# Kernel optimization log

Hardware: AMD Instinct MI355X
Metric: run time of the kernel (lower is better)

Reference implementation:

```python
import jax, jax.numpy as jnp
import numpy as np

EPS = 1e-5  # torch BatchNorm1d default eps

def _bn(y, gamma, beta):
    # training-mode BatchNorm1d over batch axis (biased variance), per timestep
    mu = jnp.mean(y, axis=0, keepdims=True)
    var = jnp.mean((y - mu) ** 2, axis=0, keepdims=True)
    return gamma * (y - mu) * jax.lax.rsqrt(var + EPS) + beta

def setup_inputs() -> dict:
    key = jax.random.key(0)
    ks = jax.random.split(key, 16)
    T, B, I, H = 512, 64, 512, 512
    s = 1.0 / np.sqrt(H)
    def w(k, shape):
        return jax.random.uniform(k, shape, jnp.float32, -s, s)
    return {
        "x": jax.random.normal(ks[0], (T, B, I), jnp.float32),
        "h0": jnp.zeros((1, B, H), jnp.float32),
        "W_z_w": w(ks[1], (H, H)), "W_z_b": w(ks[2], (H,)),
        "U_z_w": w(ks[3], (H, I)), "U_z_b": w(ks[4], (H,)),
        "W_r_w": w(ks[5], (H, H)), "W_r_b": w(ks[6], (H,)),
        "U_r_w": w(ks[7], (H, I)), "U_r_b": w(ks[8], (H,)),
        "W_h_w": w(ks[9], (H, H)), "W_h_b": w(ks[10], (H,)),
        "U_h_w": w(ks[11], (H, I)), "U_h_b": w(ks[12], (H,)),
        "bn_gamma": jnp.ones((H,), jnp.float32),
        "bn_beta": jnp.zeros((H,), jnp.float32),
    }

def reference(x, h0, W_z_w, W_z_b, U_z_w, U_z_b, W_r_w, W_r_b, U_r_w, U_r_b,
              W_h_w, W_h_b, U_h_w, U_h_b, bn_gamma, bn_beta):
    T, B, _ = x.shape
    H = h0.shape[-1]
    # precompute input projections for all timesteps (parallelizable part)
    uz = jnp.einsum('tbi,hi->tbh', x, U_z_w) + U_z_b  # [T,B,H]
    ur = jnp.einsum('tbi,hi->tbh', x, U_r_w) + U_r_b
    uh = jnp.einsum('tbi,hi->tbh', x, U_h_w) + U_h_b

    def step(h, inp):
        uz_t, ur_t, uh_t = inp
        z = jax.nn.sigmoid(h @ W_z_w.T + W_z_b + _bn(uz_t, bn_gamma, bn_beta))
        r = jax.nn.sigmoid(h @ W_r_w.T + W_r_b + _bn(ur_t, bn_gamma, bn_beta))
        new_state = jnp.tanh((r * h) @ W_h_w.T + W_h_b + _bn(uh_t, bn_gamma, bn_beta))
        h_new = (1.0 - z) * h + z * new_state
        return h_new, h_new

    _, hs = jax.lax.scan(step, h0[0], (uz, ur, uh))  # hs: [T,B,H]
    output = hs.reshape(T, B, 1, H)   # [T, B, directions=1, H]
    h_out = hs.reshape(1, T, B, H)    # faithful to torch code's final `h`
    return output, h_out
```

## Files before the change

kernel.cpp:

```cpp
#include <hip/hip_runtime.h>
#include <hip/hip_bf16.h>


using bf16x8 = __attribute__((ext_vector_type(8))) short;
using f32x4  = __attribute__((ext_vector_type(4))) float;
using fvec4  = __attribute__((ext_vector_type(4))) float;

#define NWG 32

static __device__ __forceinline__ unsigned short f2bf(float f) {
  union { float ff; unsigned int i; } v; v.ff = f;
  unsigned int x = v.i;
  x += 0x7fffu + ((x >> 16) & 1u);
  return (unsigned short)(x >> 16);
}
static __device__ __forceinline__ float h2f(unsigned short u) {
  union { unsigned short s; _Float16 h; } v; v.s = u; return (float)v.h;
}
static __device__ __forceinline__ unsigned short f2h(float f) {
  union { unsigned short s; _Float16 h; } v; v.h = (_Float16)f; return v.s;
}
static __device__ __forceinline__ float sigmoidf_(float x) {
  return 1.0f / (1.0f + __expf(-x));
}
static __device__ __forceinline__ float tanhf_(float x) {
  return 2.0f / (1.0f + __expf(-2.0f * x)) - 1.0f;
}

__global__ __launch_bounds__(256) void proj_gemm(
    const float* __restrict__ x,
    const float* __restrict__ Uz, const float* __restrict__ Ur,
    const float* __restrict__ Uh,
    const float* __restrict__ Wzb, const float* __restrict__ Wrb,
    const float* __restrict__ Whb,
    const float* __restrict__ gamma, const float* __restrict__ beta,
    unsigned short* __restrict__ ubz, unsigned short* __restrict__ ubr,
    unsigned short* __restrict__ ubh)
{
  const int mt = blockIdx.x, nt = blockIdx.y, mat = blockIdx.z;
  const float* U  = (mat == 0) ? Uz  : (mat == 1 ? Ur  : Uh);
  const float* Wb = (mat == 0) ? Wzb : (mat == 1 ? Wrb : Whb);
  unsigned short* uo = (mat == 0) ? ubz : (mat == 1 ? ubr : ubh);

  __shared__ short lA[4096];
  __shared__ short lB[4096];

  const int tid = threadIdx.x;
  const int wave = tid >> 6, lane = tid & 63;
  const int fl = lane & 15, kseg = lane >> 4;

  f32x4 acc[4];
  #pragma unroll
  for (int n = 0; n < 4; ++n) acc[n] = f32x4{0.f, 0.f, 0.f, 0.f};

  const float* xb = x + (size_t)mt * 64 * 512;
  const float* Ub = U + (size_t)nt * 64 * 512;

  for (int kt = 0; kt < 8; ++kt) {
    __syncthreads();
    #pragma unroll
    for (int c = 0; c < 2; ++c) {
      const int chunk = tid + 256 * c;
      const int row = chunk >> 3, kc = chunk & 7;
      const int lb = row * 128 + ((kc * 16) ^ ((row & 7) << 4));
      {
        const float* g = xb + (size_t)row * 512 + kt * 64 + kc * 8;
        fvec4 a0 = *(const fvec4*)g, a1 = *(const fvec4*)(g + 4);
        bf16x8 p;
        p[0] = (short)f2bf(a0[0]); p[1] = (short)f2bf(a0[1]);
        p[2] = (short)f2bf(a0[2]); p[3] = (short)f2bf(a0[3]);
        p[4] = (short)f2bf(a1[0]); p[5] = (short)f2bf(a1[1]);
        p[6] = (short)f2bf(a1[2]); p[7] = (short)f2bf(a1[3]);
        *(bf16x8*)((char*)lA + lb) = p;
      }
      {
        const float* g = Ub + (size_t)row * 512 + kt * 64 + kc * 8;
        fvec4 a0 = *(const fvec4*)g, a1 = *(const fvec4*)(g + 4);
        bf16x8 p;
        p[0] = (short)f2bf(a0[0]); p[1] = (short)f2bf(a0[1]);
        p[2] = (short)f2bf(a0[2]); p[3] = (short)f2bf(a0[3]);
        p[4] = (short)f2bf(a1[0]); p[5] = (short)f2bf(a1[1]);
        p[6] = (short)f2bf(a1[2]); p[7] = (short)f2bf(a1[3]);
        *(bf16x8*)((char*)lB + lb) = p;
      }
    }
    __syncthreads();
    #pragma unroll
    for (int kk = 0; kk < 2; ++kk) {
      const int ar = wave * 16 + fl;
      bf16x8 af = *(const bf16x8*)((char*)lA + ar * 128 +
                    ((kk * 64 + kseg * 16) ^ ((ar & 7) << 4)));
      #pragma unroll
      for (int n = 0; n < 4; ++n) {
        const int br = n * 16 + fl;
        bf16x8 bfr = *(const bf16x8*)((char*)lB + br * 128 +
                      ((kk * 64 + kseg * 16) ^ ((br & 7) << 4)));
        acc[n] = __builtin_amdgcn_mfma_f32_16x16x32_bf16(af, bfr, acc[n], 0, 0, 0);
      }
    }
  }

  float sn[4], qn[4];
  #pragma unroll
  for (int n = 0; n < 4; ++n) {
    sn[n] = acc[n][0] + acc[n][1] + acc[n][2] + acc[n][3];
    qn[n] = acc[n][0]*acc[n][0] + acc[n][1]*acc[n][1]
          + acc[n][2]*acc[n][2] + acc[n][3]*acc[n][3];
    sn[n] += __shfl_xor(sn[n], 16); qn[n] += __shfl_xor(qn[n], 16);
    sn[n] += __shfl_xor(sn[n], 32); qn[n] += __shfl_xor(qn[n], 32);
  }
  __syncthreads();
  float* sArr = (float*)lA;
  float* qArr = (float*)lB;
  if (kseg == 0) {
    #pragma unroll
    for (int n = 0; n < 4; ++n) {
      sArr[wave * 64 + n * 16 + fl] = sn[n];
      qArr[wave * 64 + n * 16 + fl] = qn[n];
    }
  }
  __syncthreads();

  const int c0 = nt * 64;
  const int r0 = mt * 64 + wave * 16 + kseg * 4;
  #pragma unroll
  for (int n = 0; n < 4; ++n) {
    const int idx = n * 16 + fl;
    const float s = sArr[idx] + sArr[64+idx] + sArr[128+idx] + sArr[192+idx];
    const float q = qArr[idx] + qArr[64+idx] + qArr[128+idx] + qArr[192+idx];
    const float mu = s * 0.015625f;
    const float rs = rsqrtf(q * 0.015625f - mu * mu + 1e-5f);
    const int col = c0 + idx;
    const float gb  = gamma[col] * rs;
    const float ofs = beta[col] + Wb[col] - gb * mu;
    #pragma unroll
    for (int i = 0; i < 4; ++i)
      uo[(size_t)(r0 + i) * 512 + col] = f2h(gb * acc[n][i] + ofs);
  }
}

__global__ __launch_bounds__(256) void gru_scan(
    const float* __restrict__ h0,
    const float* __restrict__ Wz, const float* __restrict__ Wr,
    const float* __restrict__ Wh,
    const unsigned short* __restrict__ ubz, const unsigned short* __restrict__ ubr,
    const unsigned short* __restrict__ ubh,
    unsigned short* __restrict__ hbuf, unsigned short* __restrict__ rhbuf,
    unsigned int* __restrict__ bars, float* __restrict__ out)
{
  const int wg = blockIdx.x;
  const int tid = threadIdx.x;
  const int wave = tid >> 6, lane = tid & 63;
  const int fl = lane & 15, kseg = lane >> 4;
  const int col = wg * 16 + fl;
  const int row0 = wave * 16 + kseg * 4;
  const int hrow = wave * 16 + fl;

  __shared__ short lW[24576];

  for (int c = tid; c < 3072; c += 256) {
    const int m = c >> 10, rem = c & 1023;
    const int r = rem >> 6, kc = rem & 63;
    const float* W = (m == 0) ? Wz : (m == 1 ? Wr : Wh);
    const float* g = W + (size_t)(wg * 16 + r) * 512 + kc * 8;
    bf16x8 p;
    #pragma unroll
    for (int j = 0; j < 8; ++j) p[j] = (short)f2bf(g[j]);
    *(bf16x8*)((char*)lW + m * 16384 + r * 1024 + ((kc * 16) ^ ((r & 7) << 4))) = p;
  }

  float hown[4];
  #pragma unroll
  for (int i = 0; i < 4; ++i) {
    const float v = h0[(size_t)(row0 + i) * 512 + col];
    hown[i] = v;
    hbuf[(size_t)(row0 + i) * 512 + col] = f2bf(v);
  }
  __syncthreads();
  if (tid == 0)
    __hip_atomic_fetch_add(&bars[0], 1u, __ATOMIC_RELEASE, __HIP_MEMORY_SCOPE_AGENT);

  float uzv[4], urv[4], uhv[4];
  #pragma unroll
  for (int i = 0; i < 4; ++i) {
    const size_t o = (size_t)(row0 + i) * 512 + col;
    uzv[i] = h2f(ubz[o]); urv[i] = h2f(ubr[o]); uhv[i] = h2f(ubh[o]);
  }

  for (int t = 0; t < 512; ++t) {
    if ((tid & 63) == 0) {
      while (__hip_atomic_load(&bars[2 * t], __ATOMIC_RELAXED,
                               __HIP_MEMORY_SCOPE_AGENT) < NWG)
        __builtin_amdgcn_s_sleep(1);
    }
    __builtin_amdgcn_fence(__ATOMIC_ACQUIRE, "agent");
    __syncthreads();

    bf16x8 af[16];
    #pragma unroll
    for (int kk = 0; kk < 16; ++kk)
      af[kk] = *(const bf16x8*)((const char*)hbuf + hrow * 1024 + kk * 64 + kseg * 16);

    f32x4 zacc = f32x4{0.f,0.f,0.f,0.f}, racc = f32x4{0.f,0.f,0.f,0.f};
    #pragma unroll
    for (int kk = 0; kk < 16; ++kk) {
      const int wof = (kk * 64 + kseg * 16) ^ ((fl & 7) << 4);
      bf16x8 b0 = *(const bf16x8*)((const char*)lW + fl * 1024 + wof);
      bf16x8 b1 = *(const bf16x8*)((const char*)lW + 16384 + fl * 1024 + wof);
      zacc = __builtin_amdgcn_mfma_f32_16x16x32_bf16(af[kk], b0, zacc, 0, 0, 0);
      racc = __builtin_amdgcn_mfma_f32_16x16x32_bf16(af[kk], b1, racc, 0, 0, 0);
    }

    float z4[4], r4[4];
    #pragma unroll
    for (int i = 0; i < 4; ++i) {
      z4[i] = sigmoidf_(zacc[i] + uzv[i]);
      r4[i] = sigmoidf_(racc[i] + urv[i]);
    }

    #pragma unroll
    for (int i = 0; i < 4; ++i)
      rhbuf[(size_t)(row0 + i) * 512 + col] = f2bf(r4[i] * hown[i]);

    __syncthreads();
    if (tid == 0)
      __hip_atomic_fetch_add(&bars[2*t+1], 1u, __ATOMIC_RELEASE, __HIP_MEMORY_SCOPE_AGENT);
    if ((tid & 63) == 0) {
      while (__hip_atomic_load(&bars[2*t+1], __ATOMIC_RELAXED,
                               __HIP_MEMORY_SCOPE_AGENT) < NWG)
        __builtin_amdgcn_s_sleep(1);
    }
    __builtin_amdgcn_fence(__ATOMIC_ACQUIRE, "agent");
    __syncthreads();

    #pragma unroll
    for (int kk = 0; kk < 16; ++kk)
      af[kk] = *(const bf16x8*)((const char*)rhbuf + hrow * 1024 + kk * 64 + kseg * 16);

    f32x4 hacc = f32x4{0.f,0.f,0.f,0.f};
    #pragma unroll
    for (int kk = 0; kk < 16; ++kk) {
      const int wof = (kk * 64 + kseg * 16) ^ ((fl & 7) << 4);
      bf16x8 b2 = *(const bf16x8*)((const char*)lW + 32768 + fl * 1024 + wof);
      hacc = __builtin_amdgcn_mfma_f32_16x16x32_bf16(af[kk], b2, hacc, 0, 0, 0);
    }

    float hn[4];
    #pragma unroll
    for (int i = 0; i < 4; ++i) {
      const float nb = tanhf_(hacc[i] + uhv[i]);
      hn[i] = (1.f - z4[i]) * hown[i] + z4[i] * nb;
      hown[i] = hn[i];
    }
    #pragma unroll
    for (int i = 0; i < 4; ++i)
      hbuf[(size_t)(row0 + i) * 512 + col] = f2bf(hn[i]);

    __syncthreads();
    if (tid == 0)
      __hip_atomic_fetch_add(&bars[2*t+2], 1u, __ATOMIC_RELEASE, __HIP_MEMORY_SCOPE_AGENT);

    if (t + 1 < 512) {
      const size_t tb = (size_t)(t + 1) * 64 * 512;
      #pragma unroll
      for (int i = 0; i < 4; ++i) {
        const size_t o = tb + (size_t)(row0 + i) * 512 + col;
        uzv[i] = h2f(ubz[o]); urv[i] = h2f(ubr[o]); uhv[i] = h2f(ubh[o]);
      }
    }
    {
      const size_t tb = (size_t)t * 64 * 512;
      #pragma unroll
      for (int i = 0; i < 4; ++i) {
        const size_t o = tb + (size_t)(row0 + i) * 512 + col;
        const float v = hn[i];
        out[o] = v;
        out[16777216 + o] = v;
      }
    }
  }
}

extern "C" void kernel_launch(void* const* d_in, const int* in_sizes, int n_in,
                              void* d_out, int out_size, void* d_ws, size_t ws_size,
                              hipStream_t stream) {
  (void)in_sizes; (void)n_in; (void)out_size; (void)ws_size;
  const float* x   = (const float*)d_in[0];
  const float* h0  = (const float*)d_in[1];
  const float* Wz  = (const float*)d_in[2];
  const float* Wzb = (const float*)d_in[3];
  const float* Uz  = (const float*)d_in[4];
  const float* Wr  = (const float*)d_in[6];
  const float* Wrb = (const float*)d_in[7];
  const float* Ur  = (const float*)d_in[8];
  const float* Wh  = (const float*)d_in[10];
  const float* Whb = (const float*)d_in[11];
  const float* Uh  = (const float*)d_in[12];
  const float* gam = (const float*)d_in[14];
  const float* bet = (const float*)d_in[15];
  float* out = (float*)d_out;

  char* ws = (char*)d_ws;
  unsigned int*   bars  = (unsigned int*)(ws);
  unsigned short* hbuf  = (unsigned short*)(ws + 8192);
  unsigned short* rhbuf = (unsigned short*)(ws + 8192 + 65536);
  unsigned short* uzb   = (unsigned short*)(ws + 262144);
  unsigned short* urb   = (unsigned short*)(ws + 262144 + 33554432);
  unsigned short* uhb   = (unsigned short*)(ws + 262144 + 2ll * 33554432);

  hipMemsetAsync(bars, 0, 8192, stream);

  dim3 gp(512, 8, 3);
  proj_gemm<<<gp, 256, 0, stream>>>(x, Uz, Ur, Uh, Wzb, Wrb, Whb,
                                    gam, bet, uzb, urb, uhb);
  gru_scan<<<dim3(NWG), 256, 0, stream>>>(h0, Wz, Wr, Wh, uzb, urb, uhb,
                                          hbuf, rhbuf, bars, out);
}
```

Before: 6.683 ms.

## Replace counter barriers with per-workgroup epoch flags and transpose projection layout

Grid-wide barriers built on shared atomic counters (one fetch-add and a single polling lane per wave) are replaced by per-workgroup monotonic epoch flags on separate 128-byte lines. Each wave polls all 32 flags in parallel across its lanes, without sleeping. The precomputed projection buffers are also stored batch-contiguous per column, so each scan thread loads four fp16 values with one vector load instead of four strided scalar loads. The aim is lower barrier latency on the serial time loop, at the cost of busier spinning and more polling traffic.

Result: faster. 5.739 ms (-14.1%).

```diff
diff --git a/kernel.cpp b/kernel.cpp
--- a/kernel.cpp
+++ b/kernel.cpp
@@ -5,6 +5,7 @@
 using bf16x8 = __attribute__((ext_vector_type(8))) short;
 using f32x4  = __attribute__((ext_vector_type(4))) float;
 using fvec4  = __attribute__((ext_vector_type(4))) float;
+using s16x4  = __attribute__((ext_vector_type(4))) short;
 
 #define NWG 32
 
@@ -122,7 +123,7 @@
   __syncthreads();
 
   const int c0 = nt * 64;
-  const int r0 = mt * 64 + wave * 16 + kseg * 4;
+  const int b0 = wave * 16 + kseg * 4;
   #pragma unroll
   for (int n = 0; n < 4; ++n) {
     const int idx = n * 16 + fl;
@@ -133,9 +134,11 @@
     const int col = c0 + idx;
     const float gb  = gamma[col] * rs;
     const float ofs = beta[col] + Wb[col] - gb * mu;
+    s16x4 pk;
     #pragma unroll
     for (int i = 0; i < 4; ++i)
-      uo[(size_t)(r0 + i) * 512 + col] = f2h(gb * acc[n][i] + ofs);
+      pk[i] = (short)f2h(gb * acc[n][i] + ofs);
+    *(s16x4*)(uo + ((size_t)mt * 512 + col) * 64 + b0) = pk;
   }
 }
 
@@ -146,7 +149,7 @@
     const unsigned short* __restrict__ ubz, const unsigned short* __restrict__ ubr,
     const unsigned short* __restrict__ ubh,
     unsigned short* __restrict__ hbuf, unsigned short* __restrict__ rhbuf,
-    unsigned int* __restrict__ bars, float* __restrict__ out)
+    unsigned int* __restrict__ flags, float* __restrict__ out)
 {
   const int wg = blockIdx.x;
   const int tid = threadIdx.x;
@@ -169,6 +172,14 @@
     *(bf16x8*)((char*)lW + m * 16384 + r * 1024 + ((kc * 16) ^ ((r & 7) << 4))) = p;
   }
 
+  auto wait_ev = [&](unsigned int ev) {
+    if (lane < NWG) {
+      while (__hip_atomic_load(&flags[lane << 5], __ATOMIC_RELAXED,
+                               __HIP_MEMORY_SCOPE_AGENT) < ev) {}
+    }
+    __builtin_amdgcn_fence(__ATOMIC_ACQUIRE, "agent");
+  };
+
   float hown[4];
   #pragma unroll
   for (int i = 0; i < 4; ++i) {
@@ -178,23 +189,24 @@
   }
   __syncthreads();
   if (tid == 0)
-    __hip_atomic_fetch_add(&bars[0], 1u, __ATOMIC_RELEASE, __HIP_MEMORY_SCOPE_AGENT);
+    __hip_atomic_store(&flags[wg << 5], 1u, __ATOMIC_RELEASE, __HIP_MEMORY_SCOPE_AGENT);
 
   float uzv[4], urv[4], uhv[4];
-  #pragma unroll
-  for (int i = 0; i < 4; ++i) {
-    const size_t o = (size_t)(row0 + i) * 512 + col;
-    uzv[i] = h2f(ubz[o]); urv[i] = h2f(ubr[o]); uhv[i] = h2f(ubh[o]);
+  {
+    const size_t ub = ((size_t)col) * 64 + row0;
+    s16x4 az = *(const s16x4*)(ubz + ub);
+    s16x4 ar = *(const s16x4*)(ubr + ub);
+    s16x4 ah = *(const s16x4*)(ubh + ub);
+    #pragma unroll
+    for (int i = 0; i < 4; ++i) {
+      uzv[i] = h2f((unsigned short)az[i]);
+      urv[i] = h2f((unsigned short)ar[i]);
+      uhv[i] = h2f((unsigned short)ah[i]);
+    }
   }
 
   for (int t = 0; t < 512; ++t) {
-    if ((tid & 63) == 0) {
-      while (__hip_atomic_load(&bars[2 * t], __ATOMIC_RELAXED,
-                               __HIP_MEMORY_SCOPE_AGENT) < NWG)
-        __builtin_amdgcn_s_sleep(1);
-    }
-    __builtin_amdgcn_fence(__ATOMIC_ACQUIRE, "agent");
-    __syncthreads();
+    wait_ev(2 * t + 1);
 
     bf16x8 af[16];
     #pragma unroll
@@ -224,14 +236,9 @@
 
     __syncthreads();
     if (tid == 0)
-      __hip_atomic_fetch_add(&bars[2*t+1], 1u, __ATOMIC_RELEASE, __HIP_MEMORY_SCOPE_AGENT);
-    if ((tid & 63) == 0) {
-      while (__hip_atomic_load(&bars[2*t+1], __ATOMIC_RELAXED,
-                               __HIP_MEMORY_SCOPE_AGENT) < NWG)
-        __builtin_amdgcn_s_sleep(1);
-    }
-    __builtin_amdgcn_fence(__ATOMIC_ACQUIRE, "agent");
-    __syncthreads();
+      __hip_atomic_store(&flags[wg << 5], 2u * t + 2u, __ATOMIC_RELEASE,
+                         __HIP_MEMORY_SCOPE_AGENT);
+    wait_ev(2 * t + 2);
 
     #pragma unroll
     for (int kk = 0; kk < 16; ++kk)
@@ -258,14 +265,19 @@
 
     __syncthreads();
     if (tid == 0)
-      __hip_atomic_fetch_add(&bars[2*t+2], 1u, __ATOMIC_RELEASE, __HIP_MEMORY_SCOPE_AGENT);
+      __hip_atomic_store(&flags[wg << 5], 2u * t + 3u, __ATOMIC_RELEASE,
+                         __HIP_MEMORY_SCOPE_AGENT);
 
     if (t + 1 < 512) {
-      const size_t tb = (size_t)(t + 1) * 64 * 512;
+      const size_t ub = ((size_t)(t + 1) * 512 + col) * 64 + row0;
+      s16x4 az = *(const s16x4*)(ubz + ub);
+      s16x4 ar = *(const s16x4*)(ubr + ub);
+      s16x4 ah = *(const s16x4*)(ubh + ub);
       #pragma unroll
       for (int i = 0; i < 4; ++i) {
-        const size_t o = tb + (size_t)(row0 + i) * 512 + col;
-        uzv[i] = h2f(ubz[o]); urv[i] = h2f(ubr[o]); uhv[i] = h2f(ubh[o]);
+        uzv[i] = h2f((unsigned short)az[i]);
+        urv[i] = h2f((unsigned short)ar[i]);
+        uhv[i] = h2f((unsigned short)ah[i]);
       }
     }
     {
@@ -301,18 +313,18 @@
   float* out = (float*)d_out;
 
   char* ws = (char*)d_ws;
-  unsigned int*   bars  = (unsigned int*)(ws);
+  unsigned int*   flags = (unsigned int*)(ws);
   unsigned short* hbuf  = (unsigned short*)(ws + 8192);
   unsigned short* rhbuf = (unsigned short*)(ws + 8192 + 65536);
   unsigned short* uzb   = (unsigned short*)(ws + 262144);
   unsigned short* urb   = (unsigned short*)(ws + 262144 + 33554432);
   unsigned short* uhb   = (unsigned short*)(ws + 262144 + 2ll * 33554432);
 
-  hipMemsetAsync(bars, 0, 8192, stream);
+  hipMemsetAsync(flags, 0, 8192, stream);
 
   dim3 gp(512, 8, 3);
   proj_gemm<<<gp, 256, 0, stream>>>(x, Uz, Ur, Uh, Wzb, Wrb, Whb,
                                     gam, bet, uzb, urb, uhb);
   gru_scan<<<dim3(NWG), 256, 0, stream>>>(h0, Wz, Wr, Wh, uzb, urb, uhb,
-                                          hbuf, rhbuf, bars, out);
-}
+                                          hbuf, rhbuf, flags, out);
+}
```
